# Performance work log

Measured on AMD Instinct MI355X. Metric: run time of the kernel, lower is better.

The kernel has to match this reference:

```python
import jax, jax.numpy as jnp
import numpy as np

A, I = 16, 16           # n_agents, n_items
D = A * I               # flattened bid dim
ROUNDS = 40             # sinkhorn_rounds
EPS = 0.1               # sinkhorn_epsilon
B = 32768               # batch size


def setup_inputs() -> dict:
    key = jax.random.key(0)
    ks = jax.random.split(key, 20)

    def lin(k, din, dout):
        k1, k2 = jax.random.split(k)
        s = 1.0 / np.sqrt(din)
        W = jax.random.uniform(k1, (din, dout), minval=-s, maxval=s, dtype=jnp.float32)
        b = jax.random.uniform(k2, (dout,), minval=-s, maxval=s, dtype=jnp.float32)
        return W, b

    inp = {"bids": jax.random.uniform(ks[0], (B, A, I), dtype=jnp.float32)}
    dims_a = [(D, 128), (128, 128), (128, 128), (128, D)]
    dims_p = [(D, 128), (128, 128), (128, 128), (128, A)]
    for i, (din, dout) in enumerate(dims_a):
        W, b = lin(ks[1 + i], din, dout)
        inp[f"aw{i}"] = W
        inp[f"ab{i}"] = b
    for i, (din, dout) in enumerate(dims_p):
        W, b = lin(ks[5 + i], din, dout)
        inp[f"pw{i}"] = W
        inp[f"pb{i}"] = b
    return inp


def _log_sinkhorn(log_K, log_a, log_b):
    # log_K: [B, A+1, I+1]; log_a: [A+1]; log_b: [I+1]
    def step(K, _):
        K = K + (log_a - jax.scipy.special.logsumexp(K, axis=-1))[..., :, None]
        K = K + (log_b - jax.scipy.special.logsumexp(K, axis=-2))[..., None, :]
        return K, None
    K, _ = jax.lax.scan(step, log_K, None, length=ROUNDS)
    return jnp.exp(K)


def _forward(bids, aw0, ab0, aw1, ab1, aw2, ab2, aw3, ab3,
             pw0, pb0, pw1, pb1, pw2, pb2, pw3, pb3):
    bsz = bids.shape[0]
    X = bids.reshape(bsz, D)

    h = jnp.tanh(X @ aw0 + ab0)
    h = jnp.tanh(h @ aw1 + ab1)
    h = jnp.tanh(h @ aw2 + ab2)
    augmented = h @ aw3 + ab3                     # [B, A*I]

    # bipartite matching via log-domain Sinkhorn on padded matrix
    mat = augmented.reshape(bsz, A, I)
    padded = -jnp.pad(mat, ((0, 0), (0, 1), (0, 1)))  # [B, A+1, I+1]
    # 'unit' marginals: each agent/item has mass 1, dummies absorb the rest
    log_a = jnp.log(jnp.concatenate([jnp.ones(A, jnp.float32), jnp.full((1,), float(I), jnp.float32)]))
    log_b = jnp.log(jnp.concatenate([jnp.ones(I, jnp.float32), jnp.full((1,), float(A), jnp.float32)]))
    plan = _log_sinkhorn(-padded / EPS, log_a, log_b)
    allocs = plan[:, :A, :I]                      # drop dummy row/col

    p = jnp.tanh(X @ pw0 + pb0)
    p = jnp.tanh(p @ pw1 + pb1)
    p = jnp.tanh(p @ pw2 + pb2)
    frac = jax.nn.sigmoid(p @ pw3 + pb3)          # [B, A]
    payments = frac * (allocs * bids).sum(axis=-1)
    return allocs, payments


def reference(bids, aw0, ab0, aw1, ab1, aw2, ab2, aw3, ab3,
              pw0, pb0, pw1, pb1, pw2, pb2, pw3, pb3):
    return _forward(bids, aw0, ab0, aw1, ab1, aw2, ab2, aw3, ab3,
                    pw0, pb0, pw1, pb1, pw2, pb2, pw3, pb3)
```

## Files before the change

kernel.cpp:

```cpp
#include <hip/hip_runtime.h>

#define NB 32768

typedef _Float16 half8 __attribute__((ext_vector_type(8)));
typedef float floatx4 __attribute__((ext_vector_type(4)));
typedef float floatx2 __attribute__((ext_vector_type(2)));
typedef unsigned int uint4v __attribute__((ext_vector_type(4)));

#define MFMA16(a,b,c) __builtin_amdgcn_mfma_f32_16x16x32_f16(a,b,c,0,0,0)

__device__ __forceinline__ float rcp_f(float x){ return __builtin_amdgcn_rcpf(x); }
__device__ __forceinline__ float exp2_f(float x){ return __builtin_amdgcn_exp2f(x); }
__device__ __forceinline__ float tanh_f(float x){
  float e = exp2_f(x * 2.8853900817779268f);
  return (e - 1.0f) * rcp_f(e + 1.0f);
}
__device__ __forceinline__ float sigmoid_f(float x){
  return rcp_f(1.0f + exp2_f(-1.4426950408889634f * x));
}

__device__ __forceinline__ floatx2 pk_mul2(floatx2 a, floatx2 b){
  floatx2 d; asm("v_pk_mul_f32 %0, %1, %2" : "=v"(d) : "v"(a), "v"(b)); return d;
}
__device__ __forceinline__ floatx2 pk_fma2(floatx2 a, floatx2 b, floatx2 c){
  floatx2 d; asm("v_pk_fma_f32 %0, %1, %2, %3" : "=v"(d) : "v"(a), "v"(b), "v"(c)); return d;
}

template<int CTRL>
__device__ __forceinline__ float dpp_qp(float x){
  return __builtin_bit_cast(float, __builtin_amdgcn_update_dpp(0, __builtin_bit_cast(int,x), CTRL, 0xF, 0xF, true));
}
__device__ __forceinline__ float qadd2(float x){
  x += dpp_qp<0xB1>(x);
  x += dpp_qp<0x4E>(x);
  return x;
}
__device__ __forceinline__ float qmax2(float x){
  x = fmaxf(x, dpp_qp<0xB1>(x));
  x = fmaxf(x, dpp_qp<0x4E>(x));
  return x;
}

constexpr int O_AW0H = 0;
constexpr int O_AW1H = 32768;
constexpr int O_AW2H = 49152;
constexpr int O_AW3H = 65536;
constexpr int O_PW0H = 98304;
constexpr int O_PW1H = 131072;
constexpr int O_PW2H = 147456;
constexpr int O_PW3H = 163840;
constexpr int O_AW1L = 165888;
constexpr int O_AW2L = 182272;
constexpr int O_AW3L = 198656;

struct PrepJob { const float* src; _Float16* h; _Float16* l; int nshift; int total; };
struct PrepJobs { PrepJob j[8]; };

__global__ void prep_kernel(PrepJobs js){
  const PrepJob jb = js.j[blockIdx.y];
  const int idx = blockIdx.x*256 + threadIdx.x;
  if (idx >= jb.total) return;
  const int N = 1 << jb.nshift;
  const int n = idx & (N-1);
  const int k = idx >> jb.nshift;
  const int K = jb.total >> jb.nshift;
  float w = jb.src[idx];
  _Float16 h = (_Float16)w;
  jb.h[(long)n*K + k] = h;
  if (jb.l) jb.l[(long)n*K + k] = (_Float16)(w - (float)h);
}

__device__ __forceinline__ int aaddr(int row, int col){
  int cc = (col >> 2) ^ (row & 7);
  return row*128 + (cc<<2) + (col & 3);
}

template<bool NEED_LO>
__device__ __forceinline__ void read_frag(const unsigned int* __restrict__ act,
    int row, int ks, int q, half8& ah, half8& al)
{
  const int s = row & 7;
  const int cc0 = ks*8 + q*2;
  uint4v c0 = *(const uint4v*)(act + row*128 + (((cc0  ) ^ s)<<2));
  uint4v c1 = *(const uint4v*)(act + row*128 + (((cc0+1) ^ s)<<2));
  uint4v h;
  h.x = (c0.x & 0xffffu) | (c0.y << 16);
  h.y = (c0.z & 0xffffu) | (c0.w << 16);
  h.z = (c1.x & 0xffffu) | (c1.y << 16);
  h.w = (c1.z & 0xffffu) | (c1.w << 16);
  ah = __builtin_bit_cast(half8, h);
  if constexpr (NEED_LO){
    uint4v g;
    g.x = (c0.x >> 16) | (c0.y & 0xffff0000u);
    g.y = (c0.z >> 16) | (c0.w & 0xffff0000u);
    g.z = (c1.x >> 16) | (c1.y & 0xffff0000u);
    g.w = (c1.z >> 16) | (c1.w & 0xffff0000u);
    al = __builtin_bit_cast(half8, g);
  }
}

__device__ __forceinline__ unsigned int pack_act(float v){
  _Float16 h = (_Float16)v;
  _Float16 lo = (_Float16)(v - (float)h);
  return (unsigned int)__builtin_bit_cast(unsigned short, h)
       | ((unsigned int)__builtin_bit_cast(unsigned short, lo) << 16);
}
__device__ __forceinline__ unsigned int pack_act_hi(float v){
  return (unsigned int)__builtin_bit_cast(unsigned short, (_Float16)v);
}

template<int KS, bool LO>
__device__ __forceinline__ void load_tile(
    const _Float16* __restrict__ Wh, const _Float16* __restrict__ Wl,
    int K, int nt, int l15, int q, half8* bh, half8* bl)
{
  const _Float16* bp = Wh + (nt*16 + l15)*K + q*8;
#pragma unroll
  for (int ks=0; ks<KS; ++ks) bh[ks] = *(const half8*)(bp + ks*32);
  if constexpr (LO){
    const _Float16* blp = Wl + (nt*16 + l15)*K + q*8;
#pragma unroll
    for (int ks=0; ks<KS; ++ks) bl[ks] = *(const half8*)(blp + ks*32);
  }
}

template<int KS, int PASSES, int NT, int RING, typename EPI>
__device__ __forceinline__ void mfma_stream2(
    const half8* Ah0, const half8* Al0,
    const half8* Ah1, const half8* Al1,
    const _Float16* __restrict__ Wh, const _Float16* __restrict__ Wl,
    int K, int l15, int q, EPI&& epi)
{
  half8 Bh[RING][KS], Bl[RING][KS];
  load_tile<KS,PASSES==3>(Wh, Wl, K, 0, l15, q, Bh[0], Bl[0]);
  if constexpr (RING > 2){
    if constexpr (NT > 1)
      load_tile<KS,PASSES==3>(Wh, Wl, K, 1, l15, q, Bh[1], Bl[1]);
  }
#pragma unroll
  for (int nt=0; nt<NT; ++nt){
    constexpr int PD = RING - 1;
    if (nt+PD < NT)
      load_tile<KS,PASSES==3>(Wh, Wl, K, nt+PD, l15, q, Bh[(nt+PD)%RING], Bl[(nt+PD)%RING]);
    floatx4 a0e=(floatx4)0.0f, a0o=(floatx4)0.0f;
    floatx4 a1e=(floatx4)0.0f, a1o=(floatx4)0.0f;
#pragma unroll
    for (int ks=0; ks<KS; ++ks){
      const half8 bh = Bh[nt%RING][ks];
      floatx4& c0 = (ks & 1) ? a0o : a0e;
      floatx4& c1 = (ks & 1) ? a1o : a1e;
      c0 = MFMA16(Ah0[ks], bh, c0);
      c1 = MFMA16(Ah1[ks], bh, c1);
      if constexpr (PASSES == 3){
        const half8 bl = Bl[nt%RING][ks];
        c0 = MFMA16(Al0[ks], bh, c0);
        c0 = MFMA16(Ah0[ks], bl, c0);
        c1 = MFMA16(Al1[ks], bh, c1);
        c1 = MFMA16(Ah1[ks], bl, c1);
      }
    }
    floatx4 acc0, acc1;
#pragma unroll
    for (int r=0; r<4; ++r){ acc0[r] = a0e[r] + a0o[r]; acc1[r] = a1e[r] + a1o[r]; }
    epi(nt, acc0, acc1);
  }
}

__global__ __launch_bounds__(64, 2) void fused_kernel(
  const float* __restrict__ X, const _Float16* __restrict__ WT,
  const float* __restrict__ ab0, const float* __restrict__ ab1,
  const float* __restrict__ ab2, const float* __restrict__ ab3,
  const float* __restrict__ pb0, const float* __restrict__ pb1,
  const float* __restrict__ pb2, const float* __restrict__ pb3,
  float* __restrict__ out)
{
  __shared__ unsigned int S[32*256 + 512];
  unsigned int* act_a = S;
  unsigned int* act_p = S + 4096;
  float* frac_l = (float*)(S + 8192);
  const int l = threadIdx.x, q = l>>4, l15 = l&15;
  const long rb = (long)blockIdx.x * 32;

  auto epi_act = [&](unsigned int* act, const float* bias, bool lo){
    return [=](int nt, floatx4 acc0, floatx4 acc1){
      float bb = bias[nt*16 + l15];
#pragma unroll
      for (int r=0; r<4; ++r){
        float t0 = tanh_f(acc0[r] + bb);
        act[aaddr(q*4 + r, nt*16 + l15)] = lo ? pack_act(t0) : pack_act_hi(t0);
      }
#pragma unroll
      for (int r=0; r<4; ++r){
        float t1 = tanh_f(acc1[r] + bb);
        act[aaddr(16 + q*4 + r, nt*16 + l15)] = lo ? pack_act(t1) : pack_act_hi(t1);
      }
    };
  };

  {
    half8 Xf0[8], Xf1[8];
#pragma unroll
    for (int mt=0; mt<2; ++mt){
      float4 xa[8], xb[8];
#pragma unroll
      for (int ks=0; ks<8; ++ks){
        const float* xp = X + (rb + mt*16 + l15)*256 + ks*32 + q*8;
        xa[ks] = *(const float4*)(xp);
        xb[ks] = *(const float4*)(xp + 4);
      }
      half8* Xf = mt ? Xf1 : Xf0;
#pragma unroll
      for (int ks=0; ks<8; ++ks){
        half8 h;
        h[0]=(_Float16)xa[ks].x; h[1]=(_Float16)xa[ks].y; h[2]=(_Float16)xa[ks].z; h[3]=(_Float16)xa[ks].w;
        h[4]=(_Float16)xb[ks].x; h[5]=(_Float16)xb[ks].y; h[6]=(_Float16)xb[ks].z; h[7]=(_Float16)xb[ks].w;
        Xf[ks] = h;
      }
    }
    mfma_stream2<8,1,8,2>(Xf0, Xf0, Xf1, Xf1, WT+O_AW0H, WT+O_AW0H, 256, l15, q,
                          epi_act(act_a, ab0, true));
    mfma_stream2<8,1,8,2>(Xf0, Xf0, Xf1, Xf1, WT+O_PW0H, WT+O_PW0H, 256, l15, q,
                          epi_act(act_p, pb0, false));
  }

  {
    half8 Ah0[4], Al0[4], Ah1[4], Al1[4];
#pragma unroll
    for (int ks=0; ks<4; ++ks){
      read_frag<true>(act_a, l15,      ks, q, Ah0[ks], Al0[ks]);
      read_frag<true>(act_a, 16 + l15, ks, q, Ah1[ks], Al1[ks]);
    }
    mfma_stream2<4,3,8,2>(Ah0, Al0, Ah1, Al1, WT+O_AW1H, WT+O_AW1L, 128, l15, q,
                          epi_act(act_a, ab1, true));
  }
  {
    half8 Ph0[4], Ph1[4], du;
#pragma unroll
    for (int ks=0; ks<4; ++ks){
      read_frag<false>(act_p, l15,      ks, q, Ph0[ks], du);
      read_frag<false>(act_p, 16 + l15, ks, q, Ph1[ks], du);
    }
    mfma_stream2<4,1,8,3>(Ph0, Ph0, Ph1, Ph1, WT+O_PW1H, WT+O_PW1H, 128, l15, q,
                          epi_act(act_p, pb1, false));
  }
  {
    half8 Ah0[4], Al0[4], Ah1[4], Al1[4];
#pragma unroll
    for (int ks=0; ks<4; ++ks){
      read_frag<true>(act_a, l15,      ks, q, Ah0[ks], Al0[ks]);
      read_frag<true>(act_a, 16 + l15, ks, q, Ah1[ks], Al1[ks]);
    }
    mfma_stream2<4,3,8,2>(Ah0, Al0, Ah1, Al1, WT+O_AW2H, WT+O_AW2L, 128, l15, q,
                          epi_act(act_a, ab2, true));
  }
  {
    half8 Ph0[4], Ph1[4], du;
#pragma unroll
    for (int ks=0; ks<4; ++ks){
      read_frag<false>(act_p, l15,      ks, q, Ph0[ks], du);
      read_frag<false>(act_p, 16 + l15, ks, q, Ph1[ks], du);
    }
    mfma_stream2<4,1,8,3>(Ph0, Ph0, Ph1, Ph1, WT+O_PW2H, WT+O_PW2H, 128, l15, q,
                          epi_act(act_p, pb2, false));
  }

  {
    half8 Ph0[4], Ph1[4], du;
#pragma unroll
    for (int ks=0; ks<4; ++ks){
      read_frag<false>(act_p, l15,      ks, q, Ph0[ks], du);
      read_frag<false>(act_p, 16 + l15, ks, q, Ph1[ks], du);
    }
    mfma_stream2<4,1,1,2>(Ph0, Ph0, Ph1, Ph1, WT+O_PW3H, WT+O_PW3H, 128, l15, q,
      [&](int, floatx4 acc0, floatx4 acc1){
        float bb = pb3[l15];
#pragma unroll
        for (int r=0; r<4; ++r){
          frac_l[(q*4+r)*16 + l15]      = sigmoid_f(acc0[r] + bb);
          frac_l[(16+q*4+r)*16 + l15]   = sigmoid_f(acc1[r] + bb);
        }
      });
  }
  {
    half8 Ah0[4], Al0[4], Ah1[4], Al1[4];
#pragma unroll
    for (int ks=0; ks<4; ++ks){
      read_frag<true>(act_a, l15,      ks, q, Ah0[ks], Al0[ks]);
      read_frag<true>(act_a, 16 + l15, ks, q, Ah1[ks], Al1[ks]);
    }
    float* augl = (float*)S;
#pragma unroll
    for (int hf=0; hf<2; ++hf){
      const int ncol0 = hf*128;
      mfma_stream2<4,3,8,2>(Ah0, Al0, Ah1, Al1,
                            WT+O_AW3H + hf*128*128, WT+O_AW3L + hf*128*128,
                            128, l15, q,
        [&](int nt, floatx4 acc0, floatx4 acc1){
          float bb = ab3[ncol0 + nt*16 + l15];
#pragma unroll
          for (int r=0; r<4; ++r){
            augl[(q*4+r)*256 + ncol0 + nt*16 + l15]      = acc0[r] + bb;
            augl[(16+q*4+r)*256 + ncol0 + nt*16 + l15]   = acc1[r] + bb;
          }
        });
    }
  }

  const int c = l & 3;
  const float Ssc = 14.426950408889634f;
  const float cmask = (c == 3) ? 1.0f : 0.0f;

#pragma unroll 1
  for (int mt=0; mt<2; ++mt){
    const int eL = mt*16 + (l >> 2);
    const long e = rb + eL;

    floatx2 Kp[4][8];
    floatx2 KPp[8];

    const float* ap = (const float*)S + eL*256 + 4*c;
#pragma unroll
    for (int k=0;k<8;++k){
      float4 va = *(const float4*)(ap + (2*k  )*16);
      float4 vb = *(const float4*)(ap + (2*k+1)*16);
      Kp[0][k] = (floatx2){va.x*Ssc, vb.x*Ssc};
      Kp[1][k] = (floatx2){va.y*Ssc, vb.y*Ssc};
      Kp[2][k] = (floatx2){va.z*Ssc, vb.z*Ssc};
      Kp[3][k] = (floatx2){va.w*Ssc, vb.w*Ssc};
    }

#pragma unroll
    for (int k=0;k<8;++k){
      float m0 = fmaxf(fmaxf(Kp[0][k].x,Kp[1][k].x), fmaxf(Kp[2][k].x,Kp[3][k].x));
      m0 = qmax2(fmaxf(m0, 0.0f));
      float m1 = fmaxf(fmaxf(Kp[0][k].y,Kp[1][k].y), fmaxf(Kp[2][k].y,Kp[3][k].y));
      m1 = qmax2(fmaxf(m1, 0.0f));
      Kp[0][k] = (floatx2){exp2_f(Kp[0][k].x-m0), exp2_f(Kp[0][k].y-m1)};
      Kp[1][k] = (floatx2){exp2_f(Kp[1][k].x-m0), exp2_f(Kp[1][k].y-m1)};
      Kp[2][k] = (floatx2){exp2_f(Kp[2][k].x-m0), exp2_f(Kp[2][k].y-m1)};
      Kp[3][k] = (floatx2){exp2_f(Kp[3][k].x-m0), exp2_f(Kp[3][k].y-m1)};
      KPp[k]   = (floatx2){cmask*exp2_f(-m0), cmask*exp2_f(-m1)};
    }

    float vj0=1.f, vj1=1.f, vj2=1.f, vj3=1.f;
    float v16 = cmask;
    floatx2 u2[8];
    float u16;

    for (int r=0;r<40;++r){
      floatx2 b0=(floatx2){vj0,vj0}, b1=(floatx2){vj1,vj1};
      floatx2 b2=(floatx2){vj2,vj2}, b3=(floatx2){vj3,vj3};
      floatx2 b16=(floatx2){v16,v16};
#pragma unroll
      for (int k=0;k<8;++k){
        floatx2 pp = pk_mul2(Kp[0][k], b0);
        pp = pk_fma2(Kp[1][k], b1, pp);
        pp = pk_fma2(Kp[2][k], b2, pp);
        pp = pk_fma2(Kp[3][k], b3, pp);
        pp = pk_fma2(KPp[k], b16, pp);
        float px = qadd2(pp.x);
        float py = qadd2(pp.y);
        u2[k] = (floatx2){rcp_f(px), rcp_f(py)};
      }
      {
        float p16 = (vj0+vj1) + (vj2+vj3) + cmask*v16;
        p16 = qadd2(p16);
        u16 = 16.0f * rcp_f(p16);
      }
      floatx2 t0p = pk_mul2(Kp[0][0], u2[0]);
      floatx2 t1p = pk_mul2(Kp[1][0], u2[0]);
      floatx2 t2p = pk_mul2(Kp[2][0], u2[0]);
      floatx2 t3p = pk_mul2(Kp[3][0], u2[0]);
      floatx2 tPp = pk_mul2(KPp[0],   u2[0]);
#pragma unroll
      for (int k=1;k<8;++k){
        t0p = pk_fma2(Kp[0][k], u2[k], t0p);
        t1p = pk_fma2(Kp[1][k], u2[k], t1p);
        t2p = pk_fma2(Kp[2][k], u2[k], t2p);
        t3p = pk_fma2(Kp[3][k], u2[k], t3p);
        tPp = pk_fma2(KPp[k],   u2[k], tPp);
      }
      float t0 = t0p.x + t0p.y + u16;
      float t1 = t1p.x + t1p.y + u16;
      float t2 = t2p.x + t2p.y + u16;
      float t3 = t3p.x + t3p.y + u16;
      float t16 = tPp.x + tPp.y + cmask*u16;
      vj0 = rcp_f(t0); vj1 = rcp_f(t1); vj2 = rcp_f(t2); vj3 = rcp_f(t3);
      v16 = cmask * 16.0f * rcp_f(t16 + 1e-30f + (1.0f - cmask));
    }

    float* op = out + e*256 + 4*c;
    const float* bpx = X + e*256 + 4*c;
    float pv0=0.f, pv1=0.f, pv2=0.f, pv3=0.f;
#pragma unroll
    for (int k=0;k<8;++k){
#pragma unroll
      for (int h=0;h<2;++h){
        const int i = 2*k + h;
        const float uu = h ? u2[k].y : u2[k].x;
        const float K0 = h ? Kp[0][k].y : Kp[0][k].x;
        const float K1 = h ? Kp[1][k].y : Kp[1][k].x;
        const float K2 = h ? Kp[2][k].y : Kp[2][k].x;
        const float K3 = h ? Kp[3][k].y : Kp[3][k].x;
        float4 w;
        w.x = uu*K0*vj0;
        w.y = uu*K1*vj1;
        w.z = uu*K2*vj2;
        w.w = uu*K3*vj3;
        *(float4*)(op + i*16) = w;
        float4 bb = *(const float4*)(bpx + i*16);
        float s = w.x*bb.x + w.y*bb.y + w.z*bb.z + w.w*bb.w;
        s = qadd2(s);
        if ((i>>2) == c){
          const int rr = i & 3;
          if      (rr==0) pv0 = s;
          else if (rr==1) pv1 = s;
          else if (rr==2) pv2 = s;
          else            pv3 = s;
        }
      }
    }
    const float4 fr = *(const float4*)(frac_l + eL*16 + 4*c);
    float4 pvv;
    pvv.x = pv0*fr.x; pvv.y = pv1*fr.y; pvv.z = pv2*fr.z; pvv.w = pv3*fr.w;
    *(float4*)(out + (size_t)NB*256 + e*16 + 4*c) = pvv;
  }
}

extern "C" void kernel_launch(void* const* d_in, const int* in_sizes, int n_in,
                              void* d_out, int out_size, void* d_ws, size_t ws_size,
                              hipStream_t stream)
{
  const float* bids = (const float*)d_in[0];
  const float* aw0 = (const float*)d_in[1];  const float* ab0 = (const float*)d_in[2];
  const float* aw1 = (const float*)d_in[3];  const float* ab1 = (const float*)d_in[4];
  const float* aw2 = (const float*)d_in[5];  const float* ab2 = (const float*)d_in[6];
  const float* aw3 = (const float*)d_in[7];  const float* ab3 = (const float*)d_in[8];
  const float* pw0 = (const float*)d_in[9];  const float* pb0 = (const float*)d_in[10];
  const float* pw1 = (const float*)d_in[11]; const float* pb1 = (const float*)d_in[12];
  const float* pw2 = (const float*)d_in[13]; const float* pb2 = (const float*)d_in[14];
  const float* pw3 = (const float*)d_in[15]; const float* pb3 = (const float*)d_in[16];

  _Float16* WT = (_Float16*)d_ws;

  PrepJobs js;
  js.j[0] = { aw0, WT+O_AW0H, nullptr,    7, 32768 };
  js.j[1] = { aw1, WT+O_AW1H, WT+O_AW1L,  7, 16384 };
  js.j[2] = { aw2, WT+O_AW2H, WT+O_AW2L,  7, 16384 };
  js.j[3] = { aw3, WT+O_AW3H, WT+O_AW3L,  8, 32768 };
  js.j[4] = { pw0, WT+O_PW0H, nullptr,    7, 32768 };
  js.j[5] = { pw1, WT+O_PW1H, nullptr,    7, 16384 };
  js.j[6] = { pw2, WT+O_PW2H, nullptr,    7, 16384 };
  js.j[7] = { pw3, WT+O_PW3H, nullptr,    4, 2048  };

  prep_kernel<<<dim3(128,8), 256, 0, stream>>>(js);
  fused_kernel<<<dim3(NB/32), 64, 0, stream>>>(bids, WT, ab0,ab1,ab2,ab3,
                                               pb0,pb1,pb2,pb3, (float*)d_out);
}
```

Measured before the change: 199.7 us.

## Split each 32-row block across two wavefronts sharing LDS activations

```diff
diff --git a/kernel.cpp b/kernel.cpp
--- a/kernel.cpp
+++ b/kernel.cpp
@@ -129,19 +129,19 @@
     const half8* Ah0, const half8* Al0,
     const half8* Ah1, const half8* Al1,
     const _Float16* __restrict__ Wh, const _Float16* __restrict__ Wl,
-    int K, int l15, int q, EPI&& epi)
+    int K, int nt0, int l15, int q, EPI&& epi)
 {
   half8 Bh[RING][KS], Bl[RING][KS];
-  load_tile<KS,PASSES==3>(Wh, Wl, K, 0, l15, q, Bh[0], Bl[0]);
+  load_tile<KS,PASSES==3>(Wh, Wl, K, nt0, l15, q, Bh[0], Bl[0]);
   if constexpr (RING > 2){
     if constexpr (NT > 1)
-      load_tile<KS,PASSES==3>(Wh, Wl, K, 1, l15, q, Bh[1], Bl[1]);
+      load_tile<KS,PASSES==3>(Wh, Wl, K, nt0+1, l15, q, Bh[1], Bl[1]);
   }
 #pragma unroll
   for (int nt=0; nt<NT; ++nt){
     constexpr int PD = RING - 1;
     if (nt+PD < NT)
-      load_tile<KS,PASSES==3>(Wh, Wl, K, nt+PD, l15, q, Bh[(nt+PD)%RING], Bl[(nt+PD)%RING]);
+      load_tile<KS,PASSES==3>(Wh, Wl, K, nt0+nt+PD, l15, q, Bh[(nt+PD)%RING], Bl[(nt+PD)%RING]);
     floatx4 a0e=(floatx4)0.0f, a0o=(floatx4)0.0f;
     floatx4 a1e=(floatx4)0.0f, a1o=(floatx4)0.0f;
 #pragma unroll
@@ -162,11 +162,11 @@
     floatx4 acc0, acc1;
 #pragma unroll
     for (int r=0; r<4; ++r){ acc0[r] = a0e[r] + a0o[r]; acc1[r] = a1e[r] + a1o[r]; }
-    epi(nt, acc0, acc1);
-  }
-}
-
-__global__ __launch_bounds__(64, 2) void fused_kernel(
+    epi(nt0+nt, acc0, acc1);
+  }
+}
+
+__global__ __launch_bounds__(128, 2) void fused_kernel(
   const float* __restrict__ X, const _Float16* __restrict__ WT,
   const float* __restrict__ ab0, const float* __restrict__ ab1,
   const float* __restrict__ ab2, const float* __restrict__ ab3,
@@ -178,21 +178,24 @@
   unsigned int* act_a = S;
   unsigned int* act_p = S + 4096;
   float* frac_l = (float*)(S + 8192);
-  const int l = threadIdx.x, q = l>>4, l15 = l&15;
+  const int t = threadIdx.x;
+  const int w = t >> 6;
+  const int l = t & 63, q = l>>4, l15 = l&15;
+  const int nt0 = w*4;
   const long rb = (long)blockIdx.x * 32;
 
   auto epi_act = [&](unsigned int* act, const float* bias, bool lo){
-    return [=](int nt, floatx4 acc0, floatx4 acc1){
-      float bb = bias[nt*16 + l15];
+    return [=](int ntg, floatx4 acc0, floatx4 acc1){
+      float bb = bias[ntg*16 + l15];
 #pragma unroll
       for (int r=0; r<4; ++r){
         float t0 = tanh_f(acc0[r] + bb);
-        act[aaddr(q*4 + r, nt*16 + l15)] = lo ? pack_act(t0) : pack_act_hi(t0);
+        act[aaddr(q*4 + r, ntg*16 + l15)] = lo ? pack_act(t0) : pack_act_hi(t0);
       }
 #pragma unroll
       for (int r=0; r<4; ++r){
         float t1 = tanh_f(acc1[r] + bb);
-        act[aaddr(16 + q*4 + r, nt*16 + l15)] = lo ? pack_act(t1) : pack_act_hi(t1);
+        act[aaddr(16 + q*4 + r, ntg*16 + l15)] = lo ? pack_act(t1) : pack_act_hi(t1);
       }
     };
   };
@@ -217,214 +220,193 @@
         Xf[ks] = h;
       }
     }
-    mfma_stream2<8,1,8,2>(Xf0, Xf0, Xf1, Xf1, WT+O_AW0H, WT+O_AW0H, 256, l15, q,
+    mfma_stream2<8,1,4,2>(Xf0, Xf0, Xf1, Xf1, WT+O_AW0H, WT+O_AW0H, 256, nt0, l15, q,
                           epi_act(act_a, ab0, true));
-    mfma_stream2<8,1,8,2>(Xf0, Xf0, Xf1, Xf1, WT+O_PW0H, WT+O_PW0H, 256, l15, q,
+    mfma_stream2<8,1,4,2>(Xf0, Xf0, Xf1, Xf1, WT+O_PW0H, WT+O_PW0H, 256, nt0, l15, q,
                           epi_act(act_p, pb0, false));
   }
+  __syncthreads();
+
+#pragma unroll 1
+  for (int st=0; st<2; ++st){
+    const _Float16* Wah = WT + (st ? O_AW2H : O_AW1H);
+    const _Float16* Wal = WT + (st ? O_AW2L : O_AW1L);
+    const _Float16* Wph = WT + (st ? O_PW2H : O_PW1H);
+    const float* ba = st ? ab2 : ab1;
+    const float* bp = st ? pb2 : pb1;
+    half8 Aa0[4], Ala0[4], Aa1[4], Ala1[4], Ap0[4], Ap1[4], du;
+#pragma unroll
+    for (int ks=0; ks<4; ++ks){
+      read_frag<true >(act_a, l15,      ks, q, Aa0[ks], Ala0[ks]);
+      read_frag<true >(act_a, 16 + l15, ks, q, Aa1[ks], Ala1[ks]);
+      read_frag<false>(act_p, l15,      ks, q, Ap0[ks], du);
+      read_frag<false>(act_p, 16 + l15, ks, q, Ap1[ks], du);
+    }
+    __syncthreads();
+    mfma_stream2<4,3,4,2>(Aa0, Ala0, Aa1, Ala1, Wah, Wal, 128, nt0, l15, q,
+                          epi_act(act_a, ba, true));
+    mfma_stream2<4,1,4,3>(Ap0, Ap0, Ap1, Ap1, Wph, Wph, 128, nt0, l15, q,
+                          epi_act(act_p, bp, false));
+    __syncthreads();
+  }
 
   {
-    half8 Ah0[4], Al0[4], Ah1[4], Al1[4];
+    half8 Aa0[4], Ala0[4], Aa1[4], Ala1[4], Ap0[4], Ap1[4], du;
 #pragma unroll
     for (int ks=0; ks<4; ++ks){
-      read_frag<true>(act_a, l15,      ks, q, Ah0[ks], Al0[ks]);
-      read_frag<true>(act_a, 16 + l15, ks, q, Ah1[ks], Al1[ks]);
-    }
-    mfma_stream2<4,3,8,2>(Ah0, Al0, Ah1, Al1, WT+O_AW1H, WT+O_AW1L, 128, l15, q,
-                          epi_act(act_a, ab1, true));
-  }
-  {
-    half8 Ph0[4], Ph1[4], du;
-#pragma unroll
-    for (int ks=0; ks<4; ++ks){
-      read_frag<false>(act_p, l15,      ks, q, Ph0[ks], du);
-      read_frag<false>(act_p, 16 + l15, ks, q, Ph1[ks], du);
-    }
-    mfma_stream2<4,1,8,3>(Ph0, Ph0, Ph1, Ph1, WT+O_PW1H, WT+O_PW1H, 128, l15, q,
-                          epi_act(act_p, pb1, false));
-  }
-  {
-    half8 Ah0[4], Al0[4], Ah1[4], Al1[4];
-#pragma unroll
-    for (int ks=0; ks<4; ++ks){
-      read_frag<true>(act_a, l15,      ks, q, Ah0[ks], Al0[ks]);
-      read_frag<true>(act_a, 16 + l15, ks, q, Ah1[ks], Al1[ks]);
-    }
-    mfma_stream2<4,3,8,2>(Ah0, Al0, Ah1, Al1, WT+O_AW2H, WT+O_AW2L, 128, l15, q,
-                          epi_act(act_a, ab2, true));
-  }
-  {
-    half8 Ph0[4], Ph1[4], du;
-#pragma unroll
-    for (int ks=0; ks<4; ++ks){
-      read_frag<false>(act_p, l15,      ks, q, Ph0[ks], du);
-      read_frag<false>(act_p, 16 + l15, ks, q, Ph1[ks], du);
-    }
-    mfma_stream2<4,1,8,3>(Ph0, Ph0, Ph1, Ph1, WT+O_PW2H, WT+O_PW2H, 128, l15, q,
-                          epi_act(act_p, pb2, false));
-  }
-
-  {
-    half8 Ph0[4], Ph1[4], du;
-#pragma unroll
-    for (int ks=0; ks<4; ++ks){
-      read_frag<false>(act_p, l15,      ks, q, Ph0[ks], du);
-      read_frag<false>(act_p, 16 + l15, ks, q, Ph1[ks], du);
-    }
-    mfma_stream2<4,1,1,2>(Ph0, Ph0, Ph1, Ph1, WT+O_PW3H, WT+O_PW3H, 128, l15, q,
-      [&](int, floatx4 acc0, floatx4 acc1){
-        float bb = pb3[l15];
+      read_frag<true>(act_a, l15,      ks, q, Aa0[ks], Ala0[ks]);
+      read_frag<true>(act_a, 16 + l15, ks, q, Aa1[ks], Ala1[ks]);
+    }
+    if (w == 0){
+#pragma unroll
+      for (int ks=0; ks<4; ++ks){
+        read_frag<false>(act_p, l15,      ks, q, Ap0[ks], du);
+        read_frag<false>(act_p, 16 + l15, ks, q, Ap1[ks], du);
+      }
+    }
+    __syncthreads();
+    if (w == 0){
+      mfma_stream2<4,1,1,2>(Ap0, Ap0, Ap1, Ap1, WT+O_PW3H, WT+O_PW3H, 128, 0, l15, q,
+        [&](int, floatx4 a0, floatx4 a1){
+          float bb = pb3[l15];
+#pragma unroll
+          for (int r=0; r<4; ++r){
+            frac_l[(q*4+r)*16 + l15]    = sigmoid_f(a0[r] + bb);
+            frac_l[(16+q*4+r)*16 + l15] = sigmoid_f(a1[r] + bb);
+          }
+        });
+    }
+    float* augl = (float*)S;
+    const int ncol0 = w*128;
+    mfma_stream2<4,3,8,2>(Aa0, Ala0, Aa1, Ala1,
+                          WT+O_AW3H + w*128*128, WT+O_AW3L + w*128*128,
+                          128, 0, l15, q,
+      [&](int nt, floatx4 a0, floatx4 a1){
+        float bb = ab3[ncol0 + nt*16 + l15];
 #pragma unroll
         for (int r=0; r<4; ++r){
-          frac_l[(q*4+r)*16 + l15]      = sigmoid_f(acc0[r] + bb);
-          frac_l[(16+q*4+r)*16 + l15]   = sigmoid_f(acc1[r] + bb);
+          augl[(q*4+r)*256 + ncol0 + nt*16 + l15]    = a0[r] + bb;
+          augl[(16+q*4+r)*256 + ncol0 + nt*16 + l15] = a1[r] + bb;
         }
       });
-  }
-  {
-    half8 Ah0[4], Al0[4], Ah1[4], Al1[4];
-#pragma unroll
-    for (int ks=0; ks<4; ++ks){
-      read_frag<true>(act_a, l15,      ks, q, Ah0[ks], Al0[ks]);
-      read_frag<true>(act_a, 16 + l15, ks, q, Ah1[ks], Al1[ks]);
-    }
-    float* augl = (float*)S;
-#pragma unroll
-    for (int hf=0; hf<2; ++hf){
-      const int ncol0 = hf*128;
-      mfma_stream2<4,3,8,2>(Ah0, Al0, Ah1, Al1,
-                            WT+O_AW3H + hf*128*128, WT+O_AW3L + hf*128*128,
-                            128, l15, q,
-        [&](int nt, floatx4 acc0, floatx4 acc1){
-          float bb = ab3[ncol0 + nt*16 + l15];
-#pragma unroll
-          for (int r=0; r<4; ++r){
-            augl[(q*4+r)*256 + ncol0 + nt*16 + l15]      = acc0[r] + bb;
-            augl[(16+q*4+r)*256 + ncol0 + nt*16 + l15]   = acc1[r] + bb;
-          }
-        });
-    }
+    __syncthreads();
   }
 
   const int c = l & 3;
   const float Ssc = 14.426950408889634f;
   const float cmask = (c == 3) ? 1.0f : 0.0f;
-
-#pragma unroll 1
-  for (int mt=0; mt<2; ++mt){
-    const int eL = mt*16 + (l >> 2);
-    const long e = rb + eL;
-
-    floatx2 Kp[4][8];
-    floatx2 KPp[8];
-
-    const float* ap = (const float*)S + eL*256 + 4*c;
+  const int eL = w*16 + (l >> 2);
+  const long e = rb + eL;
+
+  floatx2 Kp[4][8];
+  floatx2 KPp[8];
+
+  const float* ap = (const float*)S + eL*256 + 4*c;
+#pragma unroll
+  for (int k=0;k<8;++k){
+    float4 va = *(const float4*)(ap + (2*k  )*16);
+    float4 vb = *(const float4*)(ap + (2*k+1)*16);
+    Kp[0][k] = (floatx2){va.x*Ssc, vb.x*Ssc};
+    Kp[1][k] = (floatx2){va.y*Ssc, vb.y*Ssc};
+    Kp[2][k] = (floatx2){va.z*Ssc, vb.z*Ssc};
+    Kp[3][k] = (floatx2){va.w*Ssc, vb.w*Ssc};
+  }
+
+#pragma unroll
+  for (int k=0;k<8;++k){
+    float m0 = fmaxf(fmaxf(Kp[0][k].x,Kp[1][k].x), fmaxf(Kp[2][k].x,Kp[3][k].x));
+    m0 = qmax2(fmaxf(m0, 0.0f));
+    float m1 = fmaxf(fmaxf(Kp[0][k].y,Kp[1][k].y), fmaxf(Kp[2][k].y,Kp[3][k].y));
+    m1 = qmax2(fmaxf(m1, 0.0f));
+    Kp[0][k] = (floatx2){exp2_f(Kp[0][k].x-m0), exp2_f(Kp[0][k].y-m1)};
+    Kp[1][k] = (floatx2){exp2_f(Kp[1][k].x-m0), exp2_f(Kp[1][k].y-m1)};
+    Kp[2][k] = (floatx2){exp2_f(Kp[2][k].x-m0), exp2_f(Kp[2][k].y-m1)};
+    Kp[3][k] = (floatx2){exp2_f(Kp[3][k].x-m0), exp2_f(Kp[3][k].y-m1)};
+    KPp[k]   = (floatx2){cmask*exp2_f(-m0), cmask*exp2_f(-m1)};
+  }
+
+  float vj0=1.f, vj1=1.f, vj2=1.f, vj3=1.f;
+  float v16 = cmask;
+  floatx2 u2[8];
+  float u16;
+
+  for (int r=0;r<40;++r){
+    floatx2 b0=(floatx2){vj0,vj0}, b1=(floatx2){vj1,vj1};
+    floatx2 b2=(floatx2){vj2,vj2}, b3=(floatx2){vj3,vj3};
+    floatx2 b16=(floatx2){v16,v16};
 #pragma unroll
     for (int k=0;k<8;++k){
-      float4 va = *(const float4*)(ap + (2*k  )*16);
-      float4 vb = *(const float4*)(ap + (2*k+1)*16);
-      Kp[0][k] = (floatx2){va.x*Ssc, vb.x*Ssc};
-      Kp[1][k] = (floatx2){va.y*Ssc, vb.y*Ssc};
-      Kp[2][k] = (floatx2){va.z*Ssc, vb.z*Ssc};
-      Kp[3][k] = (floatx2){va.w*Ssc, vb.w*Ssc};
-    }
-
-#pragma unroll
-    for (int k=0;k<8;++k){
-      float m0 = fmaxf(fmaxf(Kp[0][k].x,Kp[1][k].x), fmaxf(Kp[2][k].x,Kp[3][k].x));
-      m0 = qmax2(fmaxf(m0, 0.0f));
-      float m1 = fmaxf(fmaxf(Kp[0][k].y,Kp[1][k].y), fmaxf(Kp[2][k].y,Kp[3][k].y));
-      m1 = qmax2(fmaxf(m1, 0.0f));
-      Kp[0][k] = (floatx2){exp2_f(Kp[0][k].x-m0), exp2_f(Kp[0][k].y-m1)};
-      Kp[1][k] = (floatx2){exp2_f(Kp[1][k].x-m0), exp2_f(Kp[1][k].y-m1)};
-      Kp[2][k] = (floatx2){exp2_f(Kp[2][k].x-m0), exp2_f(Kp[2][k].y-m1)};
-      Kp[3][k] = (floatx2){exp2_f(Kp[3][k].x-m0), exp2_f(Kp[3][k].y-m1)};
-      KPp[k]   = (floatx2){cmask*exp2_f(-m0), cmask*exp2_f(-m1)};
-    }
-
-    float vj0=1.f, vj1=1.f, vj2=1.f, vj3=1.f;
-    float v16 = cmask;
-    floatx2 u2[8];
-    float u16;
-
-    for (int r=0;r<40;++r){
-      floatx2 b0=(floatx2){vj0,vj0}, b1=(floatx2){vj1,vj1};
-      floatx2 b2=(floatx2){vj2,vj2}, b3=(floatx2){vj3,vj3};
-      floatx2 b16=(floatx2){v16,v16};
-#pragma unroll
-      for (int k=0;k<8;++k){
-        floatx2 pp = pk_mul2(Kp[0][k], b0);
-        pp = pk_fma2(Kp[1][k], b1, pp);
-        pp = pk_fma2(Kp[2][k], b2, pp);
-        pp = pk_fma2(Kp[3][k], b3, pp);
-        pp = pk_fma2(KPp[k], b16, pp);
-        float px = qadd2(pp.x);
-        float py = qadd2(pp.y);
-        u2[k] = (floatx2){rcp_f(px), rcp_f(py)};
-      }
-      {
-        float p16 = (vj0+vj1) + (vj2+vj3) + cmask*v16;
-        p16 = qadd2(p16);
-        u16 = 16.0f * rcp_f(p16);
-      }
-      floatx2 t0p = pk_mul2(Kp[0][0], u2[0]);
-      floatx2 t1p = pk_mul2(Kp[1][0], u2[0]);
-      floatx2 t2p = pk_mul2(Kp[2][0], u2[0]);
-      floatx2 t3p = pk_mul2(Kp[3][0], u2[0]);
-      floatx2 tPp = pk_mul2(KPp[0],   u2[0]);
-#pragma unroll
-      for (int k=1;k<8;++k){
-        t0p = pk_fma2(Kp[0][k], u2[k], t0p);
-        t1p = pk_fma2(Kp[1][k], u2[k], t1p);
-        t2p = pk_fma2(Kp[2][k], u2[k], t2p);
-        t3p = pk_fma2(Kp[3][k], u2[k], t3p);
-        tPp = pk_fma2(KPp[k],   u2[k], tPp);
-      }
-      float t0 = t0p.x + t0p.y + u16;
-      float t1 = t1p.x + t1p.y + u16;
-      float t2 = t2p.x + t2p.y + u16;
-      float t3 = t3p.x + t3p.y + u16;
-      float t16 = tPp.x + tPp.y + cmask*u16;
-      vj0 = rcp_f(t0); vj1 = rcp_f(t1); vj2 = rcp_f(t2); vj3 = rcp_f(t3);
-      v16 = cmask * 16.0f * rcp_f(t16 + 1e-30f + (1.0f - cmask));
-    }
-
-    float* op = out + e*256 + 4*c;
-    const float* bpx = X + e*256 + 4*c;
-    float pv0=0.f, pv1=0.f, pv2=0.f, pv3=0.f;
-#pragma unroll
-    for (int k=0;k<8;++k){
-#pragma unroll
-      for (int h=0;h<2;++h){
-        const int i = 2*k + h;
-        const float uu = h ? u2[k].y : u2[k].x;
-        const float K0 = h ? Kp[0][k].y : Kp[0][k].x;
-        const float K1 = h ? Kp[1][k].y : Kp[1][k].x;
-        const float K2 = h ? Kp[2][k].y : Kp[2][k].x;
-        const float K3 = h ? Kp[3][k].y : Kp[3][k].x;
-        float4 w;
-        w.x = uu*K0*vj0;
-        w.y = uu*K1*vj1;
-        w.z = uu*K2*vj2;
-        w.w = uu*K3*vj3;
-        *(float4*)(op + i*16) = w;
-        float4 bb = *(const float4*)(bpx + i*16);
-        float s = w.x*bb.x + w.y*bb.y + w.z*bb.z + w.w*bb.w;
-        s = qadd2(s);
-        if ((i>>2) == c){
-          const int rr = i & 3;
-          if      (rr==0) pv0 = s;
-          else if (rr==1) pv1 = s;
-          else if (rr==2) pv2 = s;
-          else            pv3 = s;
-        }
-      }
-    }
-    const float4 fr = *(const float4*)(frac_l + eL*16 + 4*c);
-    float4 pvv;
-    pvv.x = pv0*fr.x; pvv.y = pv1*fr.y; pvv.z = pv2*fr.z; pvv.w = pv3*fr.w;
-    *(float4*)(out + (size_t)NB*256 + e*16 + 4*c) = pvv;
-  }
+      floatx2 pp = pk_mul2(Kp[0][k], b0);
+      pp = pk_fma2(Kp[1][k], b1, pp);
+      pp = pk_fma2(Kp[2][k], b2, pp);
+      pp = pk_fma2(Kp[3][k], b3, pp);
+      pp = pk_fma2(KPp[k], b16, pp);
+      float px = qadd2(pp.x);
+      float py = qadd2(pp.y);
+      u2[k] = (floatx2){rcp_f(px), rcp_f(py)};
+    }
+    {
+      float p16 = (vj0+vj1) + (vj2+vj3) + cmask*v16;
+      p16 = qadd2(p16);
+      u16 = 16.0f * rcp_f(p16);
+    }
+    floatx2 t0p = pk_mul2(Kp[0][0], u2[0]);
+    floatx2 t1p = pk_mul2(Kp[1][0], u2[0]);
+    floatx2 t2p = pk_mul2(Kp[2][0], u2[0]);
+    floatx2 t3p = pk_mul2(Kp[3][0], u2[0]);
+    floatx2 tPp = pk_mul2(KPp[0],   u2[0]);
+#pragma unroll
+    for (int k=1;k<8;++k){
+      t0p = pk_fma2(Kp[0][k], u2[k], t0p);
+      t1p = pk_fma2(Kp[1][k], u2[k], t1p);
+      t2p = pk_fma2(Kp[2][k], u2[k], t2p);
+      t3p = pk_fma2(Kp[3][k], u2[k], t3p);
+      tPp = pk_fma2(KPp[k],   u2[k], tPp);
+    }
+    float t0 = t0p.x + t0p.y + u16;
+    float t1 = t1p.x + t1p.y + u16;
+    float t2 = t2p.x + t2p.y + u16;
+    float t3 = t3p.x + t3p.y + u16;
+    float t16 = tPp.x + tPp.y + cmask*u16;
+    vj0 = rcp_f(t0); vj1 = rcp_f(t1); vj2 = rcp_f(t2); vj3 = rcp_f(t3);
+    v16 = cmask * 16.0f * rcp_f(t16 + 1e-30f + (1.0f - cmask));
+  }
+
+  float* op = out + e*256 + 4*c;
+  const float* bpx = X + e*256 + 4*c;
+  float pv0=0.f, pv1=0.f, pv2=0.f, pv3=0.f;
+#pragma unroll
+  for (int k=0;k<8;++k){
+#pragma unroll
+    for (int h=0;h<2;++h){
+      const int i = 2*k + h;
+      const float uu = h ? u2[k].y : u2[k].x;
+      const float K0 = h ? Kp[0][k].y : Kp[0][k].x;
+      const float K1 = h ? Kp[1][k].y : Kp[1][k].x;
+      const float K2 = h ? Kp[2][k].y : Kp[2][k].x;
+      const float K3 = h ? Kp[3][k].y : Kp[3][k].x;
+      float4 wv;
+      wv.x = uu*K0*vj0;
+      wv.y = uu*K1*vj1;
+      wv.z = uu*K2*vj2;
+      wv.w = uu*K3*vj3;
+      *(float4*)(op + i*16) = wv;
+      float4 bb = *(const float4*)(bpx + i*16);
+      float s = wv.x*bb.x + wv.y*bb.y + wv.z*bb.z + wv.w*bb.w;
+      s = qadd2(s);
+      if ((i>>2) == c){
+        const int rr = i & 3;
+        if      (rr==0) pv0 = s;
+        else if (rr==1) pv1 = s;
+        else if (rr==2) pv2 = s;
+        else            pv3 = s;
+      }
+    }
+  }
+  const float4 fr = *(const float4*)(frac_l + eL*16 + 4*c);
+  float4 pvv;
+  pvv.x = pv0*fr.x; pvv.y = pv1*fr.y; pvv.z = pv2*fr.z; pvv.w = pv3*fr.w;
+  *(float4*)(out + (size_t)NB*256 + e*16 + 4*c) = pvv;
 }
 
 extern "C" void kernel_launch(void* const* d_in, const int* in_sizes, int n_in,
@@ -454,6 +436,6 @@
   js.j[7] = { pw3, WT+O_PW3H, nullptr,    4, 2048  };
 
   prep_kernel<<<dim3(128,8), 256, 0, stream>>>(js);
-  fused_kernel<<<dim3(NB/32), 64, 0, stream>>>(bids, WT, ab0,ab1,ab2,ab3,
-                                               pb0,pb1,pb2,pb3, (float*)d_out);
-}
+  fused_kernel<<<dim3(NB/32), 128, 0, stream>>>(bids, WT, ab0,ab1,ab2,ab3,
+                                                pb0,pb1,pb2,pb3, (float*)d_out);
+}
```

Result: no change. 198.7 us (-0.5%).
